# Optimization experiments

Hardware: AMD Instinct MI355X
Metric: run time of the kernel (lower is better)

## Reference

```python
import jax, jax.numpy as jnp
import numpy as np

H = 16
D_MODEL = 1024
D_K = D_MODEL // H


def setup_inputs() -> dict:
    key = jax.random.key(0)
    ks = jax.random.split(key, 8)
    B, S = 4, 2048
    query = jax.random.normal(ks[0], (B, S, D_MODEL), dtype=jnp.float32)
    key_t = jax.random.normal(ks[1], (B, S, D_MODEL), dtype=jnp.float32)
    value = jax.random.normal(ks[2], (B, S, D_MODEL), dtype=jnp.float32)
    mask = jax.random.randint(ks[3], (B, S, S), 0, 2, dtype=jnp.int32)
    sc = 1.0 / np.sqrt(D_MODEL)
    Wq = jax.random.normal(ks[4], (D_MODEL, D_MODEL), dtype=jnp.float32) * sc
    Wk = jax.random.normal(ks[5], (D_MODEL, D_MODEL), dtype=jnp.float32) * sc
    Wv = jax.random.normal(ks[6], (D_MODEL, D_MODEL), dtype=jnp.float32) * sc
    Wo = jax.random.normal(ks[7], (D_MODEL, D_MODEL), dtype=jnp.float32) * sc
    return {"query": query, "key": key_t, "value": value, "mask": mask,
            "Wq": Wq, "Wk": Wk, "Wv": Wv, "Wo": Wo}


def reference(query, key, value, mask, Wq, Wk, Wv, Wo):
    B, S, _ = query.shape
    # nn.Linear(bias=False): y = x @ W^T; then split heads -> [B,H,S,d_k]
    def proj(x, W):
        return (x @ W.T).reshape(B, S, H, D_K).transpose(0, 2, 1, 3)

    q = proj(query, Wq)
    k = proj(key, Wk)
    v = proj(value, Wv)

    m = (mask[:, None, :, :] != 0)  # [B,1,S,S] broadcast over heads
    scores = jnp.einsum('bhqd,bhkd->bhqk', q, k) / jnp.sqrt(jnp.float32(D_K))
    scores = jnp.where(m, scores, jnp.float32(-1e9))
    p_attn = jax.nn.softmax(scores, axis=-1)
    p_attn = jnp.where(m, p_attn, 0.0)
    # dropout is identity in eval mode
    x = jnp.einsum('bhqk,bhkd->bhqd', p_attn, v)
    x = x.transpose(0, 2, 1, 3).reshape(B, S, D_MODEL)
    return x @ Wo.T
```

## Files before the change

### kernel.cpp

```cpp
#include <hip/hip_runtime.h>


typedef __attribute__((ext_vector_type(8))) short frag8;
typedef __attribute__((ext_vector_type(4))) float f32x4;
typedef unsigned long long ull;

#define MFMA16(a,b,c) __builtin_amdgcn_mfma_f32_16x16x32_bf16((a),(b),(c),0,0,0)

__device__ __forceinline__ short f2bf(float f) {
  union { float f; unsigned u; } x; x.f = f;
  unsigned r = (x.u + 0x7fffu + ((x.u >> 16) & 1u)) >> 16;
  return (short)r;
}

__device__ __forceinline__ unsigned pkbf(float lo, float hi) {
  union { float f; unsigned u; } a, b;
  a.f = lo; b.f = hi;
  return __builtin_amdgcn_perm(b.u + 0x8000u, a.u + 0x8000u, 0x07060302u);
}

__device__ __forceinline__ unsigned pkbf_t(float lo, float hi) {
  union { float f; unsigned u; } a, b;
  a.f = lo; b.f = hi;
  return __builtin_amdgcn_perm(b.u, a.u, 0x07060302u);
}

__device__ __forceinline__ unsigned bit2m(unsigned word, int off) {
  unsigned r;
  asm("v_bfe_i32 %0, %1, %2, 1" : "=v"(r) : "v"(word), "v"(off));
  return r;
}
__device__ __forceinline__ unsigned mk2(unsigned word, int base) {
  return __builtin_amdgcn_perm(bit2m(word, base + 1), bit2m(word, base),
                               0x05040100u);
}

__device__ __forceinline__ void gl16(const void* g, void* l) {
  __builtin_amdgcn_global_load_lds(
      (const __attribute__((address_space(1))) unsigned*)g,
      (__attribute__((address_space(3))) unsigned*)l, 16, 0, 0);
}

__global__ __launch_bounds__(256) void cast_qkv(
    const float* __restrict__ q, const float* __restrict__ k,
    const float* __restrict__ v, short* __restrict__ qo,
    short* __restrict__ ko, short* __restrict__ vo) {
  int z = blockIdx.x >> 13;
  int i = (blockIdx.x & 8191) * 256 + threadIdx.x;
  const float* s = z == 0 ? q : z == 1 ? k : v;
  short* d = z == 0 ? qo : z == 1 ? ko : vo;
  float4 f = ((const float4*)s)[i];
  short4 o;
  o.x = f2bf(f.x); o.y = f2bf(f.y); o.z = f2bf(f.z); o.w = f2bf(f.w);
  ((short4*)d)[i] = o;
}

__global__ __launch_bounds__(256) void cast_w(
    const float* __restrict__ wq, const float* __restrict__ wk,
    const float* __restrict__ wv, const float* __restrict__ wo,
    short* __restrict__ oq, short* __restrict__ ok,
    short* __restrict__ ov, short* __restrict__ oo) {
  int z = blockIdx.x >> 10;
  int i = (blockIdx.x & 1023) * 256 + threadIdx.x;
  const float* s = z == 0 ? wq : z == 1 ? wk : z == 2 ? wv : wo;
  short* d = z == 0 ? oq : z == 1 ? ok : z == 2 ? ov : oo;
  float sc = (z == 0) ? 0.18033688011f : 1.0f;
  float4 f = ((const float4*)s)[i];
  short4 o;
  o.x = f2bf(f.x * sc); o.y = f2bf(f.y * sc);
  o.z = f2bf(f.z * sc); o.w = f2bf(f.w * sc);
  ((short4*)d)[i] = o;
}

__global__ __launch_bounds__(256) void pack_mask(
    const int* __restrict__ mask, ull* __restrict__ bits) {
  int wv = threadIdx.x >> 6, l = threadIdx.x & 63;
  size_t row = (size_t)blockIdx.x * 4 + wv;
  const int* src = mask + row * 2048;
  for (int c = 0; c < 2048; c += 64) {
    ull bl = __ballot(src[c + l] != 0);
    if (l == 0) bits[(size_t)(c >> 6) * 8192 + row] = bl;
  }
}

template <int MODE>
__device__ __forceinline__ void gemm_body(const short* __restrict__ A,
                                          const short* __restrict__ W,
                                          void* __restrict__ outp, int bid) {
  __shared__ short As[2][128 * 32];
  __shared__ short Bs[2][128 * 32];
  const int t = threadIdx.x;
  const int l = t & 63, wv = t >> 6;
  const int lg = l >> 4, lr = l & 15;
  const int wm = (wv >> 1) * 64, wn = (wv & 1) * 64;
  const int m0 = (bid >> 3) * 128;
  const int n0 = (bid & 7) * 128;

  auto stage = [&](int buf, int kt) {
    const int k0 = kt * 32;
#pragma unroll
    for (int c = 0; c < 2; ++c) {
      int idx = c * 256 + t;
      int row = idx >> 2, ch = (idx & 3) * 8;
      gl16(A + (size_t)(m0 + row) * 1024 + k0 + ch, &As[buf][idx * 8]);
      gl16(W + (size_t)(n0 + row) * 1024 + k0 + ch, &Bs[buf][idx * 8]);
    }
  };

  f32x4 acc[4][4] = {};
  stage(0, 0);
  asm volatile("s_waitcnt vmcnt(0)" ::: "memory");
  __syncthreads();
  int buf = 0;
  for (int kt = 0; kt < 32; ++kt) {
    if (kt + 1 < 32) stage(buf ^ 1, kt + 1);
    frag8 af[4], bf[4];
#pragma unroll
    for (int i = 0; i < 4; ++i) {
      af[i] = *(const frag8*)&As[buf][(wm + i * 16 + lr) * 32 + 8 * lg];
      bf[i] = *(const frag8*)&Bs[buf][(wn + i * 16 + lr) * 32 + 8 * lg];
    }
    __builtin_amdgcn_s_setprio(1);
#pragma unroll
    for (int mi = 0; mi < 4; ++mi)
#pragma unroll
      for (int ni = 0; ni < 4; ++ni)
        acc[mi][ni] = MFMA16(af[mi], bf[ni], acc[mi][ni]);
    __builtin_amdgcn_s_setprio(0);
    asm volatile("s_waitcnt vmcnt(0)" ::: "memory");
    __syncthreads();
    buf ^= 1;
  }

#pragma unroll
  for (int mi = 0; mi < 4; ++mi)
#pragma unroll
    for (int ni = 0; ni < 4; ++ni)
#pragma unroll
      for (int r = 0; r < 4; ++r) {
        int m = m0 + wm + mi * 16 + 4 * lg + r;
        int n = n0 + wn + ni * 16 + lr;
        if (MODE == 0) {
          int b = m >> 11, s = m & 2047, h = n >> 6, dk = n & 63;
          ((short*)outp)[(((size_t)b * 16 + h) * 2048 + s) * 64 + dk] =
              f2bf(acc[mi][ni][r]);
        } else {
          ((float*)outp)[(size_t)m * 1024 + n] = acc[mi][ni][r];
        }
      }
}

__global__ __launch_bounds__(256) void gemm_qkv(
    const short* __restrict__ A0, const short* __restrict__ A1,
    const short* __restrict__ A2, const short* __restrict__ W0,
    const short* __restrict__ W1, const short* __restrict__ W2,
    short* __restrict__ O0, short* __restrict__ O1, short* __restrict__ O2) {
  int wg = (blockIdx.x & 7) * 192 + (blockIdx.x >> 3);
  int z = wg >> 9, bid = wg & 511;
  const short* A = z == 0 ? A0 : z == 1 ? A1 : A2;
  const short* W = z == 0 ? W0 : z == 1 ? W1 : W2;
  short* O = z == 0 ? O0 : z == 1 ? O1 : O2;
  gemm_body<0>(A, W, O, bid);
}

__global__ __launch_bounds__(256) void gemm_o(
    const short* __restrict__ A, const short* __restrict__ W,
    float* __restrict__ O) {
  int bid = (blockIdx.x & 7) * 64 + (blockIdx.x >> 3);
  gemm_body<1>(A, W, O, bid);
}

__global__ __launch_bounds__(256) void transpose_v(
    const short* __restrict__ Vp, short* __restrict__ Vt) {
  __shared__ short lds[64 * 72];
  int bh = blockIdx.y, s0 = blockIdx.x * 64;
  int t = threadIdx.x;
  int rr = t >> 3, c0 = (t & 7) * 8;
#pragma unroll
  for (int half = 0; half < 2; ++half) {
    int r = half * 32 + rr;
    frag8 v = *(const frag8*)(Vp + ((size_t)bh * 2048 + s0 + r) * 64 + c0);
#pragma unroll
    for (int j = 0; j < 8; ++j) lds[r * 72 + c0 + j] = v[j];
  }
  __syncthreads();
#pragma unroll
  for (int half = 0; half < 2; ++half) {
    int d = half * 32 + rr;
    frag8 o;
#pragma unroll
    for (int j = 0; j < 8; ++j) o[j] = lds[(c0 + j) * 72 + d];
    *(frag8*)(Vt + ((size_t)bh * 64 + d) * 2048 + s0 + c0) = o;
  }
}

__global__ __launch_bounds__(512, 4) void attn_fwd(
    const short* __restrict__ Qp, const short* __restrict__ Kp,
    const short* __restrict__ Vt, const ull* __restrict__ mb64,
    short* __restrict__ X) {
  __shared__ __align__(16) short smem[20480];

  const int wg = (blockIdx.x & 7) * 128 + (blockIdx.x >> 3);
  const int qt = wg & 15, bh = wg >> 4;
  const int b = bh >> 4, h = bh & 15;
  const int t = threadIdx.x;
  const int l = t & 63, wv = t >> 6;
  const int lg = l >> 4, lr = l & 15;
  const int pw = wv >> 1, kvh = wv & 1;
  const int q0 = qt * 128 + pw * 32;
  const int qrow_base = b << 11;

  frag8 qf[2][2];
  const short* Qb = Qp + ((size_t)bh * 2048 + q0) * 64;
#pragma unroll
  for (int qb = 0; qb < 2; ++qb)
#pragma unroll
    for (int kc = 0; kc < 2; ++kc)
      qf[qb][kc] = *(const frag8*)(Qb + (qb * 16 + lr) * 64 + kc * 32 + 8 * lg);

  f32x4 acc[4][2] = {};
  f32x4 accl[2] = {};

  const size_t kbase = (size_t)bh * 2048 * 64;
  const size_t vbase = (size_t)bh * 64 * 2048;
  short* Pw = &smem[16384 + wv * 512];
  const int sx = lr & 7;
  const int sxp = (lr >> 1) & 3;

  frag8 ones;
#pragma unroll
  for (int j = 0; j < 8; ++j) ones[j] = (short)0x3F80;

  const int srow = t >> 3, sc = t & 7;
  const int scs = (sc ^ (srow & 7)) * 8;
  auto stageK = [&](int buf, int kt) {
    gl16(Kp + kbase + (size_t)(kt * 64 + srow) * 64 + scs,
         &smem[buf * 4096 + t * 8]);
  };
  auto stageV = [&](int buf, int kt) {
    gl16(Vt + vbase + (size_t)srow * 2048 + kt * 64 + scs,
         &smem[8192 + buf * 4096 + t * 8]);
  };

  const unsigned* mbp32 = (const unsigned*)mb64;
  const int row0 = qrow_base + q0 + lr;
  const int row1 = row0 + 16;
  unsigned mw0 = mbp32[(size_t)row0 * 2 + kvh];
  unsigned mw1 = mbp32[(size_t)row1 * 2 + kvh];

  stageK(0, 0);
  stageV(0, 0);
  asm volatile("s_waitcnt vmcnt(0)" ::: "memory");
  __syncthreads();
  int buf = 0;

  for (int kt = 0; kt < 32; ++kt) {
    unsigned mwc0 = mw0, mwc1 = mw1;
    const int nk = (kt + 1) & 31;
    mw0 = mbp32[((size_t)nk * 8192 + row0) * 2 + kvh];
    mw1 = mbp32[((size_t)nk * 8192 + row1) * 2 + kvh];
    stageV(buf ^ 1, nk);
    stageK(buf ^ 1, nk);

    const short* Kb = &smem[buf * 4096];
    f32x4 s[2][2] = {};
    __builtin_amdgcn_s_setprio(1);
#pragma unroll
    for (int nb = 0; nb < 2; ++nb) {
      const int ro = (kvh * 32 + nb * 16 + lr) * 64;
      frag8 k0 = *(const frag8*)&Kb[ro + ((0 + lg) ^ sx) * 8];
      frag8 k1 = *(const frag8*)&Kb[ro + ((4 + lg) ^ sx) * 8];
#pragma unroll
      for (int qb = 0; qb < 2; ++qb) {
        s[nb][qb] = MFMA16(k0, qf[qb][0], s[nb][qb]);
        s[nb][qb] = MFMA16(k1, qf[qb][1], s[nb][qb]);
      }
    }
    __builtin_amdgcn_s_setprio(0);

    auto softmax_store = [&](int qb, unsigned word) {
      const int q32 = lr * 32;
#pragma unroll
      for (int nb = 0; nb < 2; ++nb) {
        int base = nb * 16 + 4 * lg;
        float e0 = __builtin_amdgcn_exp2f(s[nb][qb][0]);
        float e1 = __builtin_amdgcn_exp2f(s[nb][qb][1]);
        float e2 = __builtin_amdgcn_exp2f(s[nb][qb][2]);
        float e3 = __builtin_amdgcn_exp2f(s[nb][qb][3]);
        uint2 w;
        w.x = pkbf_t(e0, e1) & mk2(word, base);
        w.y = pkbf_t(e2, e3) & mk2(word, base + 2);
        int sw = ((2 * nb + (lg >> 1)) ^ sxp) * 8 + 4 * (lg & 1);
        *(uint2*)&Pw[q32 + sw] = w;
      }
    };

    frag8 pf0, pf1;
    softmax_store(0, mwc0);
    pf0 = *(const frag8*)&Pw[lr * 32 + ((lg ^ sxp)) * 8];
    softmax_store(1, mwc1);
    pf1 = *(const frag8*)&Pw[lr * 32 + ((lg ^ sxp)) * 8];

    const short* Vb = &smem[8192 + buf * 4096];
    __builtin_amdgcn_s_setprio(1);
#pragma unroll
    for (int db = 0; db < 4; ++db) {
      frag8 vf = *(const frag8*)&Vb[(db * 16 + lr) * 64 +
                                    ((kvh * 4 + lg) ^ sx) * 8];
      acc[db][0] = MFMA16(vf, pf0, acc[db][0]);
      acc[db][1] = MFMA16(vf, pf1, acc[db][1]);
    }
    accl[0] = MFMA16(ones, pf0, accl[0]);
    accl[1] = MFMA16(ones, pf1, accl[1]);
    __builtin_amdgcn_s_setprio(0);

    asm volatile("s_waitcnt vmcnt(0)" ::: "memory");
    __syncthreads();
    buf ^= 1;
  }

  float* mf = (float*)smem;
  __syncthreads();
  if (kvh) {
#pragma unroll
    for (int i = 0; i < 8; ++i)
      *(f32x4*)&mf[pw * 2048 + i * 256 + l * 4] = acc[i >> 1][i & 1];
#pragma unroll
    for (int qb = 0; qb < 2; ++qb)
      *(f32x4*)&mf[8192 + pw * 512 + qb * 256 + l * 4] = accl[qb];
  }
  __syncthreads();
  if (!kvh) {
#pragma unroll
    for (int i = 0; i < 8; ++i) {
      f32x4 p = *(const f32x4*)&mf[pw * 2048 + i * 256 + l * 4];
      acc[i >> 1][i & 1] += p;
    }
#pragma unroll
    for (int qb = 0; qb < 2; ++qb) {
      f32x4 p = *(const f32x4*)&mf[8192 + pw * 512 + qb * 256 + l * 4];
      accl[qb] += p;
    }
#pragma unroll
    for (int qb = 0; qb < 2; ++qb) {
      float inv = 1.0f / fmaxf(accl[qb][0], 1e-30f);
      int q = q0 + qb * 16 + lr;
      size_t base = (size_t)(qrow_base + q) * 1024 + h * 64 + 4 * lg;
#pragma unroll
      for (int db = 0; db < 4; ++db) {
        uint2 o;
        o.x = pkbf(acc[db][qb][0] * inv, acc[db][qb][1] * inv);
        o.y = pkbf(acc[db][qb][2] * inv, acc[db][qb][3] * inv);
        *(uint2*)&X[base + db * 16] = o;
      }
    }
  }
}

extern "C" void kernel_launch(void* const* d_in, const int* in_sizes, int n_in,
                              void* d_out, int out_size, void* d_ws,
                              size_t ws_size, hipStream_t stream) {
  const float* q  = (const float*)d_in[0];
  const float* k  = (const float*)d_in[1];
  const float* v  = (const float*)d_in[2];
  const int*  msk = (const int*)d_in[3];
  const float* Wq = (const float*)d_in[4];
  const float* Wk = (const float*)d_in[5];
  const float* Wv = (const float*)d_in[6];
  const float* Wo = (const float*)d_in[7];

  const size_t SZ_T = 16777216;
  const size_t SZ_W = 2097152;
  char* ws = (char*)d_ws;
  short* qb  = (short*)(ws + 0 * SZ_T);
  short* kb  = (short*)(ws + 1 * SZ_T);
  short* vb  = (short*)(ws + 2 * SZ_T);
  short* Qp  = (short*)(ws + 3 * SZ_T);
  short* Kp  = (short*)(ws + 4 * SZ_T);
  short* Vp  = (short*)(ws + 5 * SZ_T);
  short* Vt  = (short*)(ws + 6 * SZ_T);
  short* X   = (short*)(ws + 7 * SZ_T);
  short* wqb = (short*)(ws + 8 * SZ_T);
  short* wkb = (short*)(ws + 8 * SZ_T + 1 * SZ_W);
  short* wvb = (short*)(ws + 8 * SZ_T + 2 * SZ_W);
  short* wob = (short*)(ws + 8 * SZ_T + 3 * SZ_W);
  void*  mb  = (void*)(ws + 8 * SZ_T + 4 * SZ_W);
  if (ws_size < 8 * SZ_T + 5 * SZ_W) return;

  cast_qkv<<<24576, 256, 0, stream>>>(q, k, v, qb, kb, vb);
  cast_w<<<4096, 256, 0, stream>>>(Wq, Wk, Wv, Wo, wqb, wkb, wvb, wob);
  gemm_qkv<<<1536, 256, 0, stream>>>(qb, kb, vb, wqb, wkb, wvb, Qp, Kp, Vp);
  pack_mask<<<2048, 256, 0, stream>>>(msk, (ull*)mb);
  transpose_v<<<dim3(32, 64), 256, 0, stream>>>(Vp, Vt);
  attn_fwd<<<1024, 512, 0, stream>>>(Qp, Kp, Vt, (const ull*)mb, X);
  gemm_o<<<512, 256, 0, stream>>>(X, wob, (float*)d_out);
}
```

Before: 252.9 us.

## Split attention work across 16 waves with 16 query rows per wave

The attention block grows from 512 to 1024 threads, and each wave now handles 16 query rows instead of 32. K and V staging is divided between the two halves of the block, and shared memory grows to hold the extra per-wave P buffers. The aim is more waves in flight and lower register pressure per wave, to better hide latency. The cost is that each K and V fragment read from LDS feeds half as many MFMAs, roughly doubling LDS read traffic per unit of compute.

```diff
diff --git a/kernel.cpp b/kernel.cpp
--- a/kernel.cpp
+++ b/kernel.cpp
@@ -194,11 +194,11 @@
   }
 }
 
-__global__ __launch_bounds__(512, 4) void attn_fwd(
+__global__ __launch_bounds__(1024, 8) void attn_fwd(
     const short* __restrict__ Qp, const short* __restrict__ Kp,
     const short* __restrict__ Vt, const ull* __restrict__ mb64,
     short* __restrict__ X) {
-  __shared__ __align__(16) short smem[20480];
+  __shared__ __align__(16) short smem[24576];
 
   const int wg = (blockIdx.x & 7) * 128 + (blockIdx.x >> 3);
   const int qt = wg & 15, bh = wg >> 4;
@@ -207,19 +207,17 @@
   const int l = t & 63, wv = t >> 6;
   const int lg = l >> 4, lr = l & 15;
   const int pw = wv >> 1, kvh = wv & 1;
-  const int q0 = qt * 128 + pw * 32;
+  const int q0 = qt * 128 + pw * 16;
   const int qrow_base = b << 11;
 
-  frag8 qf[2][2];
+  frag8 qf[2];
   const short* Qb = Qp + ((size_t)bh * 2048 + q0) * 64;
 #pragma unroll
-  for (int qb = 0; qb < 2; ++qb)
-#pragma unroll
-    for (int kc = 0; kc < 2; ++kc)
-      qf[qb][kc] = *(const frag8*)(Qb + (qb * 16 + lr) * 64 + kc * 32 + 8 * lg);
-
-  f32x4 acc[4][2] = {};
-  f32x4 accl[2] = {};
+  for (int kc = 0; kc < 2; ++kc)
+    qf[kc] = *(const frag8*)(Qb + lr * 64 + kc * 32 + 8 * lg);
+
+  f32x4 acc[4] = {};
+  f32x4 accl = {};
 
   const size_t kbase = (size_t)bh * 2048 * 64;
   const size_t vbase = (size_t)bh * 64 * 2048;
@@ -231,75 +229,64 @@
 #pragma unroll
   for (int j = 0; j < 8; ++j) ones[j] = (short)0x3F80;
 
-  const int srow = t >> 3, sc = t & 7;
+  const int st = t & 511;
+  const int srow = st >> 3, sc = st & 7;
   const int scs = (sc ^ (srow & 7)) * 8;
-  auto stageK = [&](int buf, int kt) {
-    gl16(Kp + kbase + (size_t)(kt * 64 + srow) * 64 + scs,
-         &smem[buf * 4096 + t * 8]);
-  };
-  auto stageV = [&](int buf, int kt) {
-    gl16(Vt + vbase + (size_t)srow * 2048 + kt * 64 + scs,
-         &smem[8192 + buf * 4096 + t * 8]);
+  const bool isV = t >= 512;
+  auto stageKV = [&](int buf, int kt) {
+    if (!isV)
+      gl16(Kp + kbase + (size_t)(kt * 64 + srow) * 64 + scs,
+           &smem[buf * 4096 + st * 8]);
+    else
+      gl16(Vt + vbase + (size_t)srow * 2048 + kt * 64 + scs,
+           &smem[8192 + buf * 4096 + st * 8]);
   };
 
   const unsigned* mbp32 = (const unsigned*)mb64;
   const int row0 = qrow_base + q0 + lr;
-  const int row1 = row0 + 16;
-  unsigned mw0 = mbp32[(size_t)row0 * 2 + kvh];
-  unsigned mw1 = mbp32[(size_t)row1 * 2 + kvh];
-
-  stageK(0, 0);
-  stageV(0, 0);
+  unsigned mw = mbp32[(size_t)row0 * 2 + kvh];
+
+  stageKV(0, 0);
   asm volatile("s_waitcnt vmcnt(0)" ::: "memory");
   __syncthreads();
   int buf = 0;
 
   for (int kt = 0; kt < 32; ++kt) {
-    unsigned mwc0 = mw0, mwc1 = mw1;
+    unsigned mwc = mw;
     const int nk = (kt + 1) & 31;
-    mw0 = mbp32[((size_t)nk * 8192 + row0) * 2 + kvh];
-    mw1 = mbp32[((size_t)nk * 8192 + row1) * 2 + kvh];
-    stageV(buf ^ 1, nk);
-    stageK(buf ^ 1, nk);
+    mw = mbp32[((size_t)nk * 8192 + row0) * 2 + kvh];
+    stageKV(buf ^ 1, nk);
 
     const short* Kb = &smem[buf * 4096];
-    f32x4 s[2][2] = {};
+    f32x4 s[2] = {};
     __builtin_amdgcn_s_setprio(1);
 #pragma unroll
     for (int nb = 0; nb < 2; ++nb) {
       const int ro = (kvh * 32 + nb * 16 + lr) * 64;
       frag8 k0 = *(const frag8*)&Kb[ro + ((0 + lg) ^ sx) * 8];
       frag8 k1 = *(const frag8*)&Kb[ro + ((4 + lg) ^ sx) * 8];
-#pragma unroll
-      for (int qb = 0; qb < 2; ++qb) {
-        s[nb][qb] = MFMA16(k0, qf[qb][0], s[nb][qb]);
-        s[nb][qb] = MFMA16(k1, qf[qb][1], s[nb][qb]);
-      }
+      s[nb] = MFMA16(k0, qf[0], s[nb]);
+      s[nb] = MFMA16(k1, qf[1], s[nb]);
     }
     __builtin_amdgcn_s_setprio(0);
 
-    auto softmax_store = [&](int qb, unsigned word) {
+    {
       const int q32 = lr * 32;
 #pragma unroll
       for (int nb = 0; nb < 2; ++nb) {
         int base = nb * 16 + 4 * lg;
-        float e0 = __builtin_amdgcn_exp2f(s[nb][qb][0]);
-        float e1 = __builtin_amdgcn_exp2f(s[nb][qb][1]);
-        float e2 = __builtin_amdgcn_exp2f(s[nb][qb][2]);
-        float e3 = __builtin_amdgcn_exp2f(s[nb][qb][3]);
+        float e0 = __builtin_amdgcn_exp2f(s[nb][0]);
+        float e1 = __builtin_amdgcn_exp2f(s[nb][1]);
+        float e2 = __builtin_amdgcn_exp2f(s[nb][2]);
+        float e3 = __builtin_amdgcn_exp2f(s[nb][3]);
         uint2 w;
-        w.x = pkbf_t(e0, e1) & mk2(word, base);
-        w.y = pkbf_t(e2, e3) & mk2(word, base + 2);
+        w.x = pkbf_t(e0, e1) & mk2(mwc, base);
+        w.y = pkbf_t(e2, e3) & mk2(mwc, base + 2);
         int sw = ((2 * nb + (lg >> 1)) ^ sxp) * 8 + 4 * (lg & 1);
         *(uint2*)&Pw[q32 + sw] = w;
       }
-    };
-
-    frag8 pf0, pf1;
-    softmax_store(0, mwc0);
-    pf0 = *(const frag8*)&Pw[lr * 32 + ((lg ^ sxp)) * 8];
-    softmax_store(1, mwc1);
-    pf1 = *(const frag8*)&Pw[lr * 32 + ((lg ^ sxp)) * 8];
+    }
+    frag8 pf = *(const frag8*)&Pw[lr * 32 + (lg ^ sxp) * 8];
 
     const short* Vb = &smem[8192 + buf * 4096];
     __builtin_amdgcn_s_setprio(1);
@@ -307,11 +294,9 @@
     for (int db = 0; db < 4; ++db) {
       frag8 vf = *(const frag8*)&Vb[(db * 16 + lr) * 64 +
                                     ((kvh * 4 + lg) ^ sx) * 8];
-      acc[db][0] = MFMA16(vf, pf0, acc[db][0]);
-      acc[db][1] = MFMA16(vf, pf1, acc[db][1]);
-    }
-    accl[0] = MFMA16(ones, pf0, accl[0]);
-    accl[1] = MFMA16(ones, pf1, accl[1]);
+      acc[db] = MFMA16(vf, pf, acc[db]);
+    }
+    accl = MFMA16(ones, pf, accl);
     __builtin_amdgcn_s_setprio(0);
 
     asm volatile("s_waitcnt vmcnt(0)" ::: "memory");
@@ -323,36 +308,30 @@
   __syncthreads();
   if (kvh) {
 #pragma unroll
-    for (int i = 0; i < 8; ++i)
-      *(f32x4*)&mf[pw * 2048 + i * 256 + l * 4] = acc[i >> 1][i & 1];
-#pragma unroll
-    for (int qb = 0; qb < 2; ++qb)
-      *(f32x4*)&mf[8192 + pw * 512 + qb * 256 + l * 4] = accl[qb];
+    for (int db = 0; db < 4; ++db)
+      *(f32x4*)&mf[pw * 1280 + db * 256 + l * 4] = acc[db];
+    *(f32x4*)&mf[pw * 1280 + 1024 + l * 4] = accl;
   }
   __syncthreads();
   if (!kvh) {
 #pragma unroll
-    for (int i = 0; i < 8; ++i) {
-      f32x4 p = *(const f32x4*)&mf[pw * 2048 + i * 256 + l * 4];
-      acc[i >> 1][i & 1] += p;
-    }
-#pragma unroll
-    for (int qb = 0; qb < 2; ++qb) {
-      f32x4 p = *(const f32x4*)&mf[8192 + pw * 512 + qb * 256 + l * 4];
-      accl[qb] += p;
-    }
-#pragma unroll
-    for (int qb = 0; qb < 2; ++qb) {
-      float inv = 1.0f / fmaxf(accl[qb][0], 1e-30f);
-      int q = q0 + qb * 16 + lr;
-      size_t base = (size_t)(qrow_base + q) * 1024 + h * 64 + 4 * lg;
-#pragma unroll
-      for (int db = 0; db < 4; ++db) {
-        uint2 o;
-        o.x = pkbf(acc[db][qb][0] * inv, acc[db][qb][1] * inv);
-        o.y = pkbf(acc[db][qb][2] * inv, acc[db][qb][3] * inv);
-        *(uint2*)&X[base + db * 16] = o;
-      }
+    for (int db = 0; db < 4; ++db) {
+      f32x4 p = *(const f32x4*)&mf[pw * 1280 + db * 256 + l * 4];
+      acc[db] += p;
+    }
+    {
+      f32x4 p = *(const f32x4*)&mf[pw * 1280 + 1024 + l * 4];
+      accl += p;
+    }
+    float inv = 1.0f / fmaxf(accl[0], 1e-30f);
+    int q = q0 + lr;
+    size_t base = (size_t)(qrow_base + q) * 1024 + h * 64 + 4 * lg;
+#pragma unroll
+    for (int db = 0; db < 4; ++db) {
+      uint2 o;
+      o.x = pkbf(acc[db][0] * inv, acc[db][1] * inv);
+      o.y = pkbf(acc[db][2] * inv, acc[db][3] * inv);
+      *(uint2*)&X[base + db * 16] = o;
     }
   }
 }
@@ -392,6 +371,6 @@
   gemm_qkv<<<1536, 256, 0, stream>>>(qb, kb, vb, wqb, wkb, wvb, Qp, Kp, Vp);
   pack_mask<<<2048, 256, 0, stream>>>(msk, (ull*)mb);
   transpose_v<<<dim3(32, 64), 256, 0, stream>>>(Vp, Vt);
-  attn_fwd<<<1024, 512, 0, stream>>>(Qp, Kp, Vt, (const ull*)mb, X);
+  attn_fwd<<<1024, 1024, 0, stream>>>(Qp, Kp, Vt, (const ull*)mb, X);
   gemm_o<<<512, 256, 0, stream>>>(X, wob, (float*)d_out);
 }
```

Measured after the change: 282.3 us. 1.12x slower.
